# Kernel tuning notes

Measured on AMD Instinct MI355X. Metric: run time of the kernel, lower is better.

## Reference

```python
import jax, jax.numpy as jnp
import numpy as np

B, T, E, H, V = 64, 32, 512, 512, 10000


def setup_inputs() -> dict:
    key = jax.random.key(0)
    ks = jax.random.split(key, 8)
    s_e = 1.0 / np.sqrt(E)
    s_h = 1.0 / np.sqrt(H)
    return {
        "features": jax.random.normal(ks[0], (B, E), dtype=jnp.float32),
        "captions": jax.random.randint(ks[1], (B, T), 0, V, dtype=jnp.int64),
        "embed_W": jax.random.normal(ks[2], (V, E), dtype=jnp.float32) * 0.05,
        "W_ih": jax.random.normal(ks[3], (4 * H, E), dtype=jnp.float32) * s_e,
        "W_hh": jax.random.normal(ks[4], (4 * H, H), dtype=jnp.float32) * s_h,
        "b_ih": jnp.zeros((4 * H,), dtype=jnp.float32),
        "b_hh": jnp.zeros((4 * H,), dtype=jnp.float32),
        "fc_W": jax.random.normal(ks[5], (V, H), dtype=jnp.float32) * s_h,
        "fc_b": jnp.zeros((V,), dtype=jnp.float32),
    }


def reference(features, captions, embed_W, W_ih, W_hh, b_ih, b_hh, fc_W, fc_b):
    batch = features.shape[0]
    hidden = W_hh.shape[1]
    # Build per-step LSTM inputs: t=0 uses image features, t>=1 uses embed(captions[:, t]).
    # (captions_embed[:, 0] is unused, matching the original forward.)
    cap_emb = embed_W[captions]                      # [B, T, E]
    xs = jnp.concatenate([features[:, None, :], cap_emb[:, 1:, :]], axis=1)  # [B, T, E]
    xs = jnp.swapaxes(xs, 0, 1)                      # [T, B, E] time-major for scan

    # Precompute input-to-hidden projections for all timesteps (one big GEMM).
    x_proj = jnp.einsum('tbe,ge->tbg', xs, W_ih) + b_ih + b_hh  # [T, B, 4H]

    def step(carry, xp_t):
        h, c = carry
        gates = xp_t + h @ W_hh.T                    # [B, 4H]
        i, f, g, o = jnp.split(gates, 4, axis=-1)    # PyTorch gate order i,f,g,o
        c = jax.nn.sigmoid(f) * c + jax.nn.sigmoid(i) * jnp.tanh(g)
        h = jax.nn.sigmoid(o) * jnp.tanh(c)
        return (h, c), h

    h0 = jnp.zeros((batch, hidden), dtype=features.dtype)
    c0 = jnp.zeros((batch, hidden), dtype=features.dtype)
    _, h_seq = jax.lax.scan(step, (h0, c0), x_proj)  # [T, B, H]

    # Output projection across all timesteps in one GEMM.
    logits = jnp.einsum('tbh,vh->btv', h_seq, fc_W) + fc_b  # [B, T, V]
    return logits
```

## Files before the change

### kernel.cpp

```cpp
#include <hip/hip_runtime.h>
#include <hip/hip_bf16.h>
#include <stdint.h>

typedef __attribute__((ext_vector_type(8))) short short8;
typedef __attribute__((ext_vector_type(4))) float floatx4;
typedef unsigned long long ull;

__device__ __forceinline__ floatx4 mfma_bf16(short8 a, short8 b, floatx4 c) {
  return __builtin_amdgcn_mfma_f32_16x16x32_bf16(a, b, c, 0, 0, 0);
}

__device__ __forceinline__ void async16(const void* g, void* lds) {
  __builtin_amdgcn_global_load_lds(
      (const __attribute__((address_space(1))) unsigned int*)g,
      (__attribute__((address_space(3))) unsigned int*)lds, 16, 0, 0);
}

__device__ __forceinline__ void cvt8_store(const float* __restrict__ src,
                                           __hip_bfloat16* __restrict__ dst) {
  float4 a = *(const float4*)src;
  float4 b = *(const float4*)(src + 4);
  __hip_bfloat16 t[8];
  t[0] = __float2bfloat16(a.x); t[1] = __float2bfloat16(a.y);
  t[2] = __float2bfloat16(a.z); t[3] = __float2bfloat16(a.w);
  t[4] = __float2bfloat16(b.x); t[5] = __float2bfloat16(b.y);
  t[6] = __float2bfloat16(b.z); t[7] = __float2bfloat16(b.w);
  *(uint4*)dst = *(const uint4*)t;
}

__global__ __launch_bounds__(256) void prep(
    const float* __restrict__ feat, const int* __restrict__ caps,
    const float* __restrict__ emb,  const float* __restrict__ Whh,
    const float* __restrict__ Wih,  const float* __restrict__ fcW,
    __hip_bfloat16* __restrict__ Xs,   __hip_bfloat16* __restrict__ WhhB,
    __hip_bfloat16* __restrict__ WihB, __hip_bfloat16* __restrict__ fcWB) {
  int tid = blockIdx.x * 256 + threadIdx.x;
  int r = tid >> 6;
  int ch = (tid & 63) * 8;
  const float* src;
  __hip_bfloat16* dst;
  if (r < 2048) {
    int t = r >> 6, b = r & 63;
    bool i64 = (caps[1] == 0) & (caps[3] == 0) & (caps[5] == 0) & (caps[7] == 0) &
               (caps[9] == 0) & (caps[11] == 0) & (caps[13] == 0);
    if (t == 0) {
      src = feat + (size_t)b * 512 + ch;
    } else {
      int idx = i64 ? caps[(size_t)(b * 32 + t) * 2] : caps[b * 32 + t];
      idx = idx < 0 ? 0 : (idx > 9999 ? 9999 : idx);
      src = emb + (size_t)idx * 512 + ch;
    }
    dst = Xs + (size_t)r * 512 + ch;
  } else if (r < 4096) {
    src = Whh + (size_t)(r - 2048) * 512 + ch;  dst = WhhB + (size_t)(r - 2048) * 512 + ch;
  } else if (r < 6144) {
    src = Wih + (size_t)(r - 4096) * 512 + ch;  dst = WihB + (size_t)(r - 4096) * 512 + ch;
  } else {
    src = fcW + (size_t)(r - 6144) * 512 + ch;  dst = fcWB + (size_t)(r - 6144) * 512 + ch;
  }
  cvt8_store(src, dst);
}

__global__ __launch_bounds__(256) void gemm_nt(
    const __hip_bfloat16* __restrict__ A,
    const void* __restrict__ Bv,
    const float* __restrict__ b1,
    const float* __restrict__ b2,
    float* __restrict__ outF,
    int Nrows, int ldc, int mode, int bf16B) {
  const int K = 512;
  __shared__ __align__(16) __hip_bfloat16 As[128 * 32];
  __shared__ __align__(16) __hip_bfloat16 Bs[128 * 32];
  const int tid = threadIdx.x;
  const int ib = blockIdx.x, jb = blockIdx.y;
  const int w = tid >> 6, l = tid & 63, lr = l & 15, lq = l >> 4;
  const int wr = (w & 1) * 64, wc = (w >> 1) * 64;
  floatx4 acc[4][4] = {};
  for (int kt = 0; kt < 16; ++kt) {
    const int k0 = kt * 32;
#pragma unroll
    for (int it = 0; it < 2; ++it) {
      const int flat0 = it * 256 + w * 64;
      const int flat = flat0 + l;
      const int row = flat >> 2, c8 = (flat & 3) * 8;
      async16(A + (size_t)(ib * 128 + row) * K + k0 + c8, As + flat0 * 8);
      int rb = jb * 128 + row;
      if (rb > Nrows - 1) rb = Nrows - 1;
      if (bf16B) {
        async16((const __hip_bfloat16*)Bv + (size_t)rb * K + k0 + c8, Bs + flat0 * 8);
      } else {
        cvt8_store((const float*)Bv + (size_t)rb * K + k0 + c8, Bs + flat * 8);
      }
    }
    __syncthreads();
    short8 af[4], bfr[4];
#pragma unroll
    for (int mt = 0; mt < 4; ++mt)
      af[mt] = *(const short8*)(As + (wr + mt * 16 + lr) * 32 + lq * 8);
#pragma unroll
    for (int nt = 0; nt < 4; ++nt)
      bfr[nt] = *(const short8*)(Bs + (wc + nt * 16 + lr) * 32 + lq * 8);
#pragma unroll
    for (int mt = 0; mt < 4; ++mt)
#pragma unroll
      for (int nt = 0; nt < 4; ++nt)
        acc[mt][nt] = mfma_bf16(af[mt], bfr[nt], acc[mt][nt]);
    __syncthreads();
  }
#pragma unroll
  for (int mt = 0; mt < 4; ++mt) {
#pragma unroll
    for (int nt = 0; nt < 4; ++nt) {
      int col = jb * 128 + wc + nt * 16 + lr;
      if (col < Nrows) {
        float bias = b1[col] + (b2 ? b2[col] : 0.f);
#pragma unroll
        for (int r = 0; r < 4; ++r) {
          int row = ib * 128 + wr + mt * 16 + lq * 4 + r;
          size_t orow = mode ? (size_t)((row & 63) * 32 + (row >> 6)) : (size_t)row;
          outF[orow * ldc + col] = acc[mt][nt][r] + bias;
        }
      }
    }
  }
}

__global__ __launch_bounds__(256, 1) void lstm_seq(
    const float* __restrict__ xp,
    const __hip_bfloat16* __restrict__ Whh,
    __hip_bfloat16* __restrict__ hseq,
    unsigned* __restrict__ cnt) {
  const int bg = blockIdx.x >> 4;
  const int ug = blockIdx.x & 15;
  const int tid = threadIdx.x;
  const int w = tid >> 6, l = tid & 63, lr = l & 15, lq = l >> 4;
  const int bl = tid >> 5, uu = tid & 31;
  __shared__ float gbuf[4][16][32];
  __shared__ __align__(8) __hip_bfloat16 hbuf[16][32];
  float c0 = 0.f, c1 = 0.f;

  short8 B0[16], B1[16];
  {
    const __hip_bfloat16* w0 = Whh + (size_t)(w * 512 + ug * 32 + lr) * 512 + lq * 8;
    const __hip_bfloat16* w1 = w0 + (size_t)16 * 512;
#pragma unroll
    for (int kk = 0; kk < 16; ++kk) {
      B0[kk] = *(const short8*)(w0 + kk * 32);
      B1[kk] = *(const short8*)(w1 + kk * 32);
    }
  }

  for (int t = 0; t < 32; ++t) {
    const float* xr0 = xp + ((size_t)t * 64 + bg * 16 + bl) * 2048 + ug * 32 + uu;
    const float* xr1 = xr0 + (size_t)8 * 2048;
    float xi0 = xr0[0], xf0 = xr0[512], xg0 = xr0[1024], xo0 = xr0[1536];
    float xi1 = xr1[0], xf1 = xr1[512], xg1 = xr1[1024], xo1 = xr1[1536];

    floatx4 a0 = {}, a1 = {};
    if (t > 0) {
      if (tid == 0) {
        const unsigned* f = cnt + ((t - 1) * 4 + bg) * 32;
        while (__hip_atomic_load(f, __ATOMIC_RELAXED, __HIP_MEMORY_SCOPE_AGENT) < 16u)
          __builtin_amdgcn_s_sleep(1);
      }
      __syncthreads();
      const ull* hp = (const ull*)(hseq + (size_t)((t - 1) * 64 + bg * 16 + lr) * 512);
#pragma unroll
      for (int kk = 0; kk < 16; ++kk) {
        union { ull u[2]; short8 v; } hv;
        hv.u[0] = __hip_atomic_load(hp + kk * 8 + lq * 2,
                                    __ATOMIC_RELAXED, __HIP_MEMORY_SCOPE_AGENT);
        hv.u[1] = __hip_atomic_load(hp + kk * 8 + lq * 2 + 1,
                                    __ATOMIC_RELAXED, __HIP_MEMORY_SCOPE_AGENT);
        a0 = mfma_bf16(hv.v, B0[kk], a0);
        a1 = mfma_bf16(hv.v, B1[kk], a1);
      }
    }
#pragma unroll
    for (int r = 0; r < 4; ++r) {
      gbuf[w][lq * 4 + r][lr] = a0[r];
      gbuf[w][lq * 4 + r][16 + lr] = a1[r];
    }
    __syncthreads();
    {
      float gi = gbuf[0][bl][uu] + xi0, gf = gbuf[1][bl][uu] + xf0;
      float gg = gbuf[2][bl][uu] + xg0, go = gbuf[3][bl][uu] + xo0;
      float c = 1.f / (1.f + __expf(-gf)) * c0 + 1.f / (1.f + __expf(-gi)) * tanhf(gg);
      c0 = c;
      hbuf[bl][uu] = __float2bfloat16(1.f / (1.f + __expf(-go)) * tanhf(c));
    }
    {
      float gi = gbuf[0][bl + 8][uu] + xi1, gf = gbuf[1][bl + 8][uu] + xf1;
      float gg = gbuf[2][bl + 8][uu] + xg1, go = gbuf[3][bl + 8][uu] + xo1;
      float c = 1.f / (1.f + __expf(-gf)) * c1 + 1.f / (1.f + __expf(-gi)) * tanhf(gg);
      c1 = c;
      hbuf[bl + 8][uu] = __float2bfloat16(1.f / (1.f + __expf(-go)) * tanhf(c));
    }
    __syncthreads();
    if (tid < 128) {
      int r = tid >> 3, g = tid & 7;
      ull val = *(const ull*)(&hbuf[r][g * 4]);
      ull* dst = (ull*)(hseq + (size_t)(t * 64 + bg * 16 + r) * 512 + ug * 32) + g;
      __hip_atomic_store(dst, val, __ATOMIC_RELAXED, __HIP_MEMORY_SCOPE_AGENT);
    }
    __builtin_amdgcn_s_waitcnt(0);
    __syncthreads();
    if (tid == 0)
      __hip_atomic_fetch_add(cnt + (t * 4 + bg) * 32, 1u,
                             __ATOMIC_RELAXED, __HIP_MEMORY_SCOPE_AGENT);
  }
}

extern "C" void kernel_launch(void* const* d_in, const int* in_sizes, int n_in,
                              void* d_out, int out_size, void* d_ws, size_t ws_size,
                              hipStream_t stream) {
  const float* feat = (const float*)d_in[0];
  const int* caps   = (const int*)d_in[1];
  const float* emb  = (const float*)d_in[2];
  const float* Wih  = (const float*)d_in[3];
  const float* Whh  = (const float*)d_in[4];
  const float* bih  = (const float*)d_in[5];
  const float* bhh  = (const float*)d_in[6];
  const float* fcW  = (const float*)d_in[7];
  const float* fcb  = (const float*)d_in[8];
  float* out = (float*)d_out;

  const size_t MB = 1048576;
  char* ws = (char*)d_ws;
  __hip_bfloat16* Xs   = (__hip_bfloat16*)(ws);
  __hip_bfloat16* WhhB = (__hip_bfloat16*)(ws + 2 * MB);
  __hip_bfloat16* WihB = (__hip_bfloat16*)(ws + 4 * MB);
  float*          xprj = (float*)(ws + 6 * MB);
  __hip_bfloat16* hseq = (__hip_bfloat16*)(ws + 22 * MB);
  unsigned*       cnt  = (unsigned*)(ws + 24 * MB);
  __hip_bfloat16* fcWB = (__hip_bfloat16*)(ws + 24 * MB + 16384);
  const size_t need = 24 * MB + 16384 + (size_t)10000 * 512 * 2;
  const int doFc = (ws_size >= need);

  hipMemsetAsync(cnt, 0, 16384, stream);

  int rows = doFc ? 16144 : 6144;
  prep<<<rows / 4, 256, 0, stream>>>(feat, caps, emb, Whh, Wih, fcW,
                                     Xs, WhhB, WihB, fcWB);

  gemm_nt<<<dim3(16, 16), 256, 0, stream>>>(Xs, WihB, bih, bhh, xprj,
                                            2048, 2048, 0, 1);

  lstm_seq<<<64, 256, 0, stream>>>(xprj, WhhB, hseq, cnt);

  if (doFc)
    gemm_nt<<<dim3(16, 79), 256, 0, stream>>>(hseq, fcWB, fcb, nullptr, out,
                                              10000, 10000, 1, 1);
  else
    gemm_nt<<<dim3(16, 79), 256, 0, stream>>>(hseq, fcW, fcb, nullptr, out,
                                              10000, 10000, 1, 0);
}
```

Measured before the change: 355.3 us.

## Replace counter barrier with tagged h packets and swap GEMM grid order

The LSTM recurrence no longer signals each step through a per-batch-group atomic counter that one thread spins on. Each hidden value pair is now stored as a 64-bit packet holding the bf16 data plus a timestep tag. Consumers poll their own packets and start the MFMA for each chunk as soon as that chunk is valid, which removes the memset, the s_waitcnt, the extra barriers and the fetch_add from the critical path. The packet buffer reuses workspace already consumed by the input-projection GEMM, and it relies on leftover tags from earlier data never matching by chance. The GEMM block index mapping is also swapped so that consecutive blocks walk the vocabulary dimension, which may change L2 reuse of the A tiles.

```diff
diff --git a/kernel.cpp b/kernel.cpp
--- a/kernel.cpp
+++ b/kernel.cpp
@@ -72,7 +72,7 @@
   __shared__ __align__(16) __hip_bfloat16 As[128 * 32];
   __shared__ __align__(16) __hip_bfloat16 Bs[128 * 32];
   const int tid = threadIdx.x;
-  const int ib = blockIdx.x, jb = blockIdx.y;
+  const int jb = blockIdx.x, ib = blockIdx.y;
   const int w = tid >> 6, l = tid & 63, lr = l & 15, lq = l >> 4;
   const int wr = (w & 1) * 64, wc = (w >> 1) * 64;
   floatx4 acc[4][4] = {};
@@ -129,14 +129,15 @@
     const float* __restrict__ xp,
     const __hip_bfloat16* __restrict__ Whh,
     __hip_bfloat16* __restrict__ hseq,
-    unsigned* __restrict__ cnt) {
+    ull* __restrict__ hpk) {
   const int bg = blockIdx.x >> 4;
   const int ug = blockIdx.x & 15;
   const int tid = threadIdx.x;
   const int w = tid >> 6, l = tid & 63, lr = l & 15, lq = l >> 4;
   const int bl = tid >> 5, uu = tid & 31;
+  const int pr = tid >> 4, pp = tid & 15;
   __shared__ float gbuf[4][16][32];
-  __shared__ __align__(8) __hip_bfloat16 hbuf[16][32];
+  __shared__ __align__(16) __hip_bfloat16 hbuf[16][32];
   float c0 = 0.f, c1 = 0.f;
 
   short8 B0[16], B1[16];
@@ -158,22 +159,39 @@
 
     floatx4 a0 = {}, a1 = {};
     if (t > 0) {
-      if (tid == 0) {
-        const unsigned* f = cnt + ((t - 1) * 4 + bg) * 32;
-        while (__hip_atomic_load(f, __ATOMIC_RELAXED, __HIP_MEMORY_SCOPE_AGENT) < 16u)
-          __builtin_amdgcn_s_sleep(1);
-      }
-      __syncthreads();
-      const ull* hp = (const ull*)(hseq + (size_t)((t - 1) * 64 + bg * 16 + lr) * 512);
-#pragma unroll
-      for (int kk = 0; kk < 16; ++kk) {
-        union { ull u[2]; short8 v; } hv;
-        hv.u[0] = __hip_atomic_load(hp + kk * 8 + lq * 2,
-                                    __ATOMIC_RELAXED, __HIP_MEMORY_SCOPE_AGENT);
-        hv.u[1] = __hip_atomic_load(hp + kk * 8 + lq * 2 + 1,
-                                    __ATOMIC_RELAXED, __HIP_MEMORY_SCOPE_AGENT);
-        a0 = mfma_bf16(hv.v, B0[kk], a0);
-        a1 = mfma_bf16(hv.v, B1[kk], a1);
+      const unsigned tagv = (unsigned)t;
+      const ull* pb = hpk + ((((size_t)(t - 1) * 4 + bg) * 16 * 16 + lr) * 16) + lq * 4;
+      ull q[4][4];
+#pragma unroll
+      for (int g = 0; g < 4; ++g)
+#pragma unroll
+        for (int j = 0; j < 4; ++j)
+          q[g][j] = __hip_atomic_load(pb + g * 256 + j,
+                                      __ATOMIC_RELAXED, __HIP_MEMORY_SCOPE_AGENT);
+      for (int cg = 0; cg < 16; ++cg) {
+        const int g = cg & 3;
+        for (;;) {
+          bool ok = ((unsigned)(q[g][0] >> 32) == tagv) &
+                    ((unsigned)(q[g][1] >> 32) == tagv) &
+                    ((unsigned)(q[g][2] >> 32) == tagv) &
+                    ((unsigned)(q[g][3] >> 32) == tagv);
+          if (__all((int)ok)) break;
+#pragma unroll
+          for (int j = 0; j < 4; ++j)
+            q[g][j] = __hip_atomic_load(pb + cg * 256 + j,
+                                        __ATOMIC_RELAXED, __HIP_MEMORY_SCOPE_AGENT);
+        }
+        union { unsigned i[4]; short8 v; } av;
+#pragma unroll
+        for (int j = 0; j < 4; ++j) av.i[j] = (unsigned)q[g][j];
+        a0 = mfma_bf16(av.v, B0[cg], a0);
+        a1 = mfma_bf16(av.v, B1[cg], a1);
+        if (cg + 4 < 16) {
+#pragma unroll
+          for (int j = 0; j < 4; ++j)
+            q[g][j] = __hip_atomic_load(pb + (cg + 4) * 256 + j,
+                                        __ATOMIC_RELAXED, __HIP_MEMORY_SCOPE_AGENT);
+        }
       }
     }
 #pragma unroll
@@ -197,17 +215,17 @@
       hbuf[bl + 8][uu] = __float2bfloat16(1.f / (1.f + __expf(-go)) * tanhf(c));
     }
     __syncthreads();
-    if (tid < 128) {
-      int r = tid >> 3, g = tid & 7;
-      ull val = *(const ull*)(&hbuf[r][g * 4]);
-      ull* dst = (ull*)(hseq + (size_t)(t * 64 + bg * 16 + r) * 512 + ug * 32) + g;
-      __hip_atomic_store(dst, val, __ATOMIC_RELAXED, __HIP_MEMORY_SCOPE_AGENT);
-    }
-    __builtin_amdgcn_s_waitcnt(0);
-    __syncthreads();
-    if (tid == 0)
-      __hip_atomic_fetch_add(cnt + (t * 4 + bg) * 32, 1u,
-                             __ATOMIC_RELAXED, __HIP_MEMORY_SCOPE_AGENT);
+    {
+      unsigned lo = *(const unsigned*)&hbuf[pr][pp * 2];
+      ull pkt = (ull)lo | ((ull)(unsigned)(t + 1) << 32);
+      ull* dst = hpk + ((((size_t)t * 4 + bg) * 16 + ug) * 16 + pr) * 16 + pp;
+      __hip_atomic_store(dst, pkt, __ATOMIC_RELAXED, __HIP_MEMORY_SCOPE_AGENT);
+    }
+    if (tid < 64) {
+      int r = tid >> 2, seg = tid & 3;
+      *(uint4*)(hseq + (size_t)(t * 64 + bg * 16 + r) * 512 + ug * 32 + seg * 8) =
+          *(const uint4*)&hbuf[r][seg * 8];
+    }
   }
 }
 
@@ -228,16 +246,14 @@
   const size_t MB = 1048576;
   char* ws = (char*)d_ws;
   __hip_bfloat16* Xs   = (__hip_bfloat16*)(ws);
-  __hip_bfloat16* WhhB = (__hip_bfloat16*)(ws + 2 * MB);
-  __hip_bfloat16* WihB = (__hip_bfloat16*)(ws + 4 * MB);
+  __hip_bfloat16* WihB = (__hip_bfloat16*)(ws + 2 * MB);
+  ull*            hpk  = (ull*)(ws);
+  __hip_bfloat16* WhhB = (__hip_bfloat16*)(ws + 4 * MB);
   float*          xprj = (float*)(ws + 6 * MB);
   __hip_bfloat16* hseq = (__hip_bfloat16*)(ws + 22 * MB);
-  unsigned*       cnt  = (unsigned*)(ws + 24 * MB);
-  __hip_bfloat16* fcWB = (__hip_bfloat16*)(ws + 24 * MB + 16384);
-  const size_t need = 24 * MB + 16384 + (size_t)10000 * 512 * 2;
+  __hip_bfloat16* fcWB = (__hip_bfloat16*)(ws + 24 * MB);
+  const size_t need = 24 * MB + (size_t)10000 * 512 * 2;
   const int doFc = (ws_size >= need);
-
-  hipMemsetAsync(cnt, 0, 16384, stream);
 
   int rows = doFc ? 16144 : 6144;
   prep<<<rows / 4, 256, 0, stream>>>(feat, caps, emb, Whh, Wih, fcW,
@@ -246,12 +262,12 @@
   gemm_nt<<<dim3(16, 16), 256, 0, stream>>>(Xs, WihB, bih, bhh, xprj,
                                             2048, 2048, 0, 1);
 
-  lstm_seq<<<64, 256, 0, stream>>>(xprj, WhhB, hseq, cnt);
+  lstm_seq<<<64, 256, 0, stream>>>(xprj, WhhB, hseq, hpk);
 
   if (doFc)
-    gemm_nt<<<dim3(16, 79), 256, 0, stream>>>(hseq, fcWB, fcb, nullptr, out,
+    gemm_nt<<<dim3(79, 16), 256, 0, stream>>>(hseq, fcWB, fcb, nullptr, out,
                                               10000, 10000, 1, 1);
   else
-    gemm_nt<<<dim3(16, 79), 256, 0, stream>>>(hseq, fcW, fcb, nullptr, out,
+    gemm_nt<<<dim3(79, 16), 256, 0, stream>>>(hseq, fcW, fcb, nullptr, out,
                                               10000, 10000, 1, 0);
 }
```

Result: slower. 457.5 us (+28.7%).
